# Kernel optimization log

Hardware: AMD Instinct MI355X
Metric: run time of the kernel (lower is better)

The kernel has to match this reference:

```python
import jax, jax.numpy as jnp
import numpy as np

N_HEADS = 32
D_MODEL = 1024
D_K = D_MODEL // N_HEADS  # 32; must equal N_HEADS for the module's broadcast to be valid
B, S = 2, 2048


def setup_inputs() -> dict:
    key = jax.random.key(0)
    ks = jax.random.split(key, 6)
    s = 0.02
    return {
        "x": jax.random.normal(ks[0], (B, S, D_MODEL), jnp.float32),
        "Wq": jax.random.normal(ks[1], (D_MODEL, D_MODEL), jnp.float32) * s,
        "bq": jnp.zeros((D_MODEL,), jnp.float32),
        "Wk": jax.random.normal(ks[2], (D_MODEL, D_K), jnp.float32) * s,
        "bk": jnp.zeros((D_K,), jnp.float32),
        "Wv": jax.random.normal(ks[3], (D_MODEL, D_K), jnp.float32) * s,
        "bv": jnp.zeros((D_K,), jnp.float32),
        "Wo": jax.random.normal(ks[4], (D_MODEL, D_MODEL), jnp.float32) * s,
        "bo": jnp.zeros((D_MODEL,), jnp.float32),
    }


def reference(x, Wq, bq, Wk, bk, Wv, bv, Wo, bo):
    b, s_len, d = x.shape
    q = x @ Wq + bq                 # (B,S,D)
    k = x @ Wk + bk                 # (B,S,D_K) -- single shared K head (MQA)
    v = x @ Wv + bv                 # (B,S,D_K)
    # Faithful to torch: view(B,S,d_k,n_heads).transpose(1,2) -> (B, D_K, S, N_HEADS)
    # The 'a' axis (size D_K) acts as the broadcast batch axis paired with the
    # expanded K/V head axis (size N_HEADS); valid because D_K == N_HEADS.
    q = q.reshape(b, s_len, D_K, N_HEADS).transpose(0, 2, 1, 3)  # (B,A,S,H)
    scores = jnp.einsum('bash,bth->bast', q, k) / jnp.sqrt(jnp.float32(D_K))  # (B,A,S,S)
    w = jax.nn.softmax(scores, axis=-1)
    out = jnp.einsum('bast,bte->base', w, v)  # (B,A,S,D_K)
    out = out.transpose(0, 2, 1, 3).reshape(b, s_len, d)  # (B,S,D)
    return out @ Wo + bo
```

## Files before the change

kernel.cpp:

```cpp
#include <hip/hip_runtime.h>
#include <cstdint>
#include <cstddef>

typedef unsigned short u16;
typedef unsigned int u32;
typedef __attribute__((ext_vector_type(8))) short short8;
typedef __attribute__((ext_vector_type(4))) float f32x4;

#define S_LEN 2048
#define NBATCH 2
#define DM 1024
#define DK 32
#define NH 32
#define M_ROWS 4096
#define SCALE 0.17677669529663687f

__device__ __forceinline__ u16 bf16_rne(float f) {
  u32 u = __float_as_uint(f);
  u32 r = (u + 0x7FFFu + ((u >> 16) & 1u)) >> 16;
  return (u16)r;
}
__device__ __forceinline__ void split2(float x, u16& hi, u16& lo) {
  u32 u = __float_as_uint(x);
  hi = (u16)(u >> 16);
  float hif = __uint_as_float(u & 0xFFFF0000u);
  lo = bf16_rne(x - hif);
}
__device__ __forceinline__ u32 pack2(float lo, float hi) {
  return (u32)bf16_rne(lo) | ((u32)bf16_rne(hi) << 16);
}

__global__ __launch_bounds__(256)
void split_x(const float* __restrict__ X, u16* __restrict__ Hi,
             u16* __restrict__ Lo) {
  const size_t i0 = ((size_t)blockIdx.x * 256 + threadIdx.x) * 8;
  const float4 v0 = *(const float4*)(X + i0);
  const float4 v1 = *(const float4*)(X + i0 + 4);
  const float f[8] = {v0.x, v0.y, v0.z, v0.w, v1.x, v1.y, v1.z, v1.w};
  u16 h[8], l[8];
#pragma unroll
  for (int e = 0; e < 8; ++e) split2(f[e], h[e], l[e]);
  uint4 hv, lv;
  hv.x = h[0] | ((u32)h[1] << 16); hv.y = h[2] | ((u32)h[3] << 16);
  hv.z = h[4] | ((u32)h[5] << 16); hv.w = h[6] | ((u32)h[7] << 16);
  lv.x = l[0] | ((u32)l[1] << 16); lv.y = l[2] | ((u32)l[3] << 16);
  lv.z = l[4] | ((u32)l[5] << 16); lv.w = l[6] | ((u32)l[7] << 16);
  *(uint4*)(Hi + i0) = hv;
  *(uint4*)(Lo + i0) = lv;
}

__global__ __launch_bounds__(256)
void tsplit(const float* __restrict__ W, u16* __restrict__ Thi,
            u16* __restrict__ Tlo) {
  __shared__ float tile[32][33];
  const int k0 = blockIdx.x * 32, n0 = blockIdx.y * 32;
  const int tx = threadIdx.x & 31, ty = threadIdx.x >> 5;
#pragma unroll
  for (int i = 0; i < 4; ++i)
    tile[ty + 8 * i][tx] = W[(size_t)(k0 + ty + 8 * i) * DM + n0 + tx];
  __syncthreads();
#pragma unroll
  for (int i = 0; i < 4; ++i) {
    const float v = tile[tx][ty + 8 * i];
    u16 h, l;
    split2(v, h, l);
    const size_t d = (size_t)(n0 + ty + 8 * i) * DM + k0 + tx;
    Thi[d] = h;
    Tlo[d] = l;
  }
}

template <int QMODE>
__global__ __launch_bounds__(256)
void gemm_mfma(const u16* __restrict__ Ahi, const u16* __restrict__ Alo,
               const u16* __restrict__ Bhi, const u16* __restrict__ Blo,
               const float* __restrict__ bias, float* __restrict__ C,
               u16* __restrict__ Ohi, u16* __restrict__ Olo) {
  __shared__ u16 lds[4][8][64][8];
  const int t = threadIdx.x;
  const int bid = blockIdx.x;
  const int swz = (bid & 7) * 32 + (bid >> 3);
  const int m0 = (swz & 31) * 128;
  const int n0 = (swz >> 5) * 128;

  const int r = t >> 1, h = t & 1;
  const size_t arow = (size_t)(m0 + r) * DM;
  const size_t brow = (size_t)(n0 + r) * DM;
  const int koff = 16 * h;
  const int mt = r >> 4;
  const int l0w = 32 * h + (r & 15);

  const int wr = t >> 7, wc = (t >> 6) & 1, l = t & 63;

  f32x4 acc[4][4];
#pragma unroll
  for (int i = 0; i < 4; ++i)
#pragma unroll
    for (int j = 0; j < 4; ++j) acc[i][j] = (f32x4){0.f, 0.f, 0.f, 0.f};

  int4 rah0, rah1, ral0, ral1, rbh0, rbh1, rbl0, rbl1;
#define GLOAD(k0)                                        \
  do {                                                   \
    const u16* pa = Ahi + arow + (k0) + koff;            \
    rah0 = *(const int4*)pa;                             \
    rah1 = *(const int4*)(pa + 8);                       \
    const u16* pal = Alo + arow + (k0) + koff;           \
    ral0 = *(const int4*)pal;                            \
    ral1 = *(const int4*)(pal + 8);                      \
    const u16* pb = Bhi + brow + (k0) + koff;            \
    rbh0 = *(const int4*)pb;                             \
    rbh1 = *(const int4*)(pb + 8);                       \
    const u16* pbl = Blo + brow + (k0) + koff;           \
    rbl0 = *(const int4*)pbl;                            \
    rbl1 = *(const int4*)(pbl + 8);                      \
  } while (0)

  GLOAD(0);

  for (int ks = 0; ks < 32; ++ks) {
    *(int4*)&lds[0][mt][l0w][0] = rah0;
    *(int4*)&lds[0][mt][l0w + 16][0] = rah1;
    *(int4*)&lds[1][mt][l0w][0] = ral0;
    *(int4*)&lds[1][mt][l0w + 16][0] = ral1;
    *(int4*)&lds[2][mt][l0w][0] = rbh0;
    *(int4*)&lds[2][mt][l0w + 16][0] = rbh1;
    *(int4*)&lds[3][mt][l0w][0] = rbl0;
    *(int4*)&lds[3][mt][l0w + 16][0] = rbl1;
    __syncthreads();
    if (ks < 31) GLOAD((ks + 1) * 32);

    short8 ah[4], al[4], bh[4], bl[4];
#pragma unroll
    for (int i = 0; i < 4; ++i) {
      ah[i] = *(const short8*)&lds[0][wr * 4 + i][l][0];
      al[i] = *(const short8*)&lds[1][wr * 4 + i][l][0];
      bh[i] = *(const short8*)&lds[2][wc * 4 + i][l][0];
      bl[i] = *(const short8*)&lds[3][wc * 4 + i][l][0];
    }
#pragma unroll
    for (int i = 0; i < 4; ++i)
#pragma unroll
      for (int j = 0; j < 4; ++j) {
        acc[i][j] = __builtin_amdgcn_mfma_f32_16x16x32_bf16(ah[i], bh[j],
                                                            acc[i][j], 0, 0, 0);
        acc[i][j] = __builtin_amdgcn_mfma_f32_16x16x32_bf16(ah[i], bl[j],
                                                            acc[i][j], 0, 0, 0);
        acc[i][j] = __builtin_amdgcn_mfma_f32_16x16x32_bf16(al[i], bh[j],
                                                            acc[i][j], 0, 0, 0);
      }
    __syncthreads();
  }
#undef GLOAD

  const int lcol = l & 15;
  float bj[4];
#pragma unroll
  for (int j = 0; j < 4; ++j) bj[j] = bias[n0 + wc * 64 + j * 16 + lcol];
#pragma unroll
  for (int i = 0; i < 4; ++i) {
    const int row0 = m0 + wr * 64 + i * 16 + (l >> 4) * 4;
#pragma unroll
    for (int j = 0; j < 4; ++j) {
      const int coln = n0 + wc * 64 + j * 16 + lcol;
#pragma unroll
      for (int q = 0; q < 4; ++q) {
        const float val = acc[i][j][q] + bj[j];
        if constexpr (QMODE == 0) {
          C[(size_t)(row0 + q) * DM + coln] = val;
        } else {
          u16 hh, ll;
          split2(val * SCALE, hh, ll);
          Ohi[(size_t)(row0 + q) * DM + coln] = hh;
          Olo[(size_t)(row0 + q) * DM + coln] = ll;
        }
      }
    }
  }
}

__global__ __launch_bounds__(256)
void kv_proj(const float* __restrict__ X, const float* __restrict__ Wk,
             const float* __restrict__ bk, const float* __restrict__ Wv,
             const float* __restrict__ bv, u16* __restrict__ Khi,
             u16* __restrict__ Klo, u16* __restrict__ Vthi,
             u16* __restrict__ Vtlo) {
  const int col = threadIdx.x & 63;
  const int rr = threadIdx.x >> 6;
  const int row = blockIdx.x * 4 + rr;
  const float* __restrict__ xr = X + (size_t)row * DM;
  const bool isK = col < DK;
  const int cc = isK ? col : col - DK;
  const float* __restrict__ w = (isK ? Wk : Wv) + cc;
  float acc = isK ? bk[cc] : bv[cc];
#pragma unroll 8
  for (int k = 0; k < DM; ++k) acc = fmaf(xr[k], w[(size_t)k * DK], acc);
  u16 h, l;
  split2(acc, h, l);
  if (isK) {
    Khi[(size_t)row * DK + cc] = h;
    Klo[(size_t)row * DK + cc] = l;
  } else {
    const size_t d =
        (size_t)(row >> 11) * DK * S_LEN + (size_t)cc * S_LEN + (row & 2047);
    Vthi[d] = h;
    Vtlo[d] = l;
  }
}

__global__ __launch_bounds__(256, 4)
void flash_mfma(const u16* __restrict__ Qhi, const u16* __restrict__ Qlo,
                const u16* __restrict__ Khi, const u16* __restrict__ Klo,
                const u16* __restrict__ Vthi, const u16* __restrict__ Vtlo,
                u16* __restrict__ Ohi, u16* __restrict__ Olo) {
  __shared__ u16 stg[4][2][64][8];
  __shared__ u16 plds[4][2][64][8];
  const int a = blockIdx.y, b = blockIdx.z;
  const int tid = threadIdx.x;
  const int wv = tid >> 6, l = tid & 63;
  const int lq = l & 15, lc = l >> 4;
  const int q0w = blockIdx.x * 128 + wv * 32;

  short8 qh[2], ql[2];
#pragma unroll
  for (int mt = 0; mt < 2; ++mt) {
    const size_t off =
        (size_t)(b * S_LEN + q0w + mt * 16 + lq) * DM + a * DK + lc * 8;
    qh[mt] = *(const short8*)(Qhi + off);
    ql[mt] = *(const short8*)(Qlo + off);
  }

  f32x4 oacc[2][2];
#pragma unroll
  for (int mt = 0; mt < 2; ++mt)
#pragma unroll
    for (int et = 0; et < 2; ++et) oacc[mt][et] = (f32x4){0.f, 0.f, 0.f, 0.f};
  float lsum[2] = {0.f, 0.f};

  const int g = tid & 127, sr = g >> 2, sc = g & 3;
  const u16* __restrict__ srcK =
      (tid < 128 ? Khi : Klo) + (size_t)(b * S_LEN + sr) * DK + sc * 8;
  const u16* __restrict__ srcV = (tid < 128 ? Vthi : Vtlo) +
                                 (size_t)b * DK * S_LEN + (size_t)sr * S_LEN +
                                 sc * 8;
  u16* const dstK = &stg[tid >> 7][sr >> 4][(sc << 4) | (sr & 15)][0];
  u16* const dstV = &stg[2 + (tid >> 7)][sr >> 4][(sc << 4) | (sr & 15)][0];

  int4 regK = *(const int4*)srcK;
  int4 regV = *(const int4*)srcV;

  for (int it = 0; it < 64; ++it) {
    *(int4*)dstK = regK;
    *(int4*)dstV = regV;
    __syncthreads();
    if (it < 63) {
      const int t0n = (it + 1) * 32;
      regK = *(const int4*)(srcK + (size_t)t0n * DK);
      regV = *(const int4*)(srcV + t0n);
    }
    short8 kh[2], kl[2], vh[2], vl[2];
#pragma unroll
    for (int tt = 0; tt < 2; ++tt) {
      kh[tt] = *(const short8*)&stg[0][tt][l][0];
      kl[tt] = *(const short8*)&stg[1][tt][l][0];
      vh[tt] = *(const short8*)&stg[2][tt][l][0];
      vl[tt] = *(const short8*)&stg[3][tt][l][0];
    }
#pragma unroll
    for (int mt = 0; mt < 2; ++mt) {
      f32x4 s0 = (f32x4){0.f, 0.f, 0.f, 0.f};
      f32x4 s1 = (f32x4){0.f, 0.f, 0.f, 0.f};
      s0 = __builtin_amdgcn_mfma_f32_16x16x32_bf16(kh[0], qh[mt], s0, 0, 0, 0);
      s0 = __builtin_amdgcn_mfma_f32_16x16x32_bf16(kh[0], ql[mt], s0, 0, 0, 0);
      s0 = __builtin_amdgcn_mfma_f32_16x16x32_bf16(kl[0], qh[mt], s0, 0, 0, 0);
      s1 = __builtin_amdgcn_mfma_f32_16x16x32_bf16(kh[1], qh[mt], s1, 0, 0, 0);
      s1 = __builtin_amdgcn_mfma_f32_16x16x32_bf16(kh[1], ql[mt], s1, 0, 0, 0);
      s1 = __builtin_amdgcn_mfma_f32_16x16x32_bf16(kl[1], qh[mt], s1, 0, 0, 0);
      const float e0 = __expf(s0[0]), e1 = __expf(s0[1]);
      const float e2 = __expf(s0[2]), e3 = __expf(s0[3]);
      const float e4 = __expf(s1[0]), e5 = __expf(s1[1]);
      const float e6 = __expf(s1[2]), e7 = __expf(s1[3]);
      lsum[mt] += ((e0 + e1) + (e2 + e3)) + ((e4 + e5) + (e6 + e7));
      const u32 pA = pack2(e0, e1), pB = pack2(e2, e3);
      const u32 pC = pack2(e4, e5), pD = pack2(e6, e7);
      const int fl1 = ((lc >> 1) << 4) | lq;
      const int fl2 = (((lc >> 1) + 2) << 4) | lq;
      *(uint2*)&plds[wv][mt][fl1][(lc & 1) * 4] = make_uint2(pA, pB);
      *(uint2*)&plds[wv][mt][fl2][(lc & 1) * 4] = make_uint2(pC, pD);
    }
    __syncthreads();
#pragma unroll
    for (int mt = 0; mt < 2; ++mt) {
      const short8 pf = *(const short8*)&plds[wv][mt][l][0];
      oacc[mt][0] = __builtin_amdgcn_mfma_f32_16x16x32_bf16(pf, vh[0],
                                                            oacc[mt][0], 0, 0, 0);
      oacc[mt][0] = __builtin_amdgcn_mfma_f32_16x16x32_bf16(pf, vl[0],
                                                            oacc[mt][0], 0, 0, 0);
      oacc[mt][1] = __builtin_amdgcn_mfma_f32_16x16x32_bf16(pf, vh[1],
                                                            oacc[mt][1], 0, 0, 0);
      oacc[mt][1] = __builtin_amdgcn_mfma_f32_16x16x32_bf16(pf, vl[1],
                                                            oacc[mt][1], 0, 0, 0);
    }
  }

#pragma unroll
  for (int mt = 0; mt < 2; ++mt) {
    float s = lsum[mt];
    s += __shfl_xor(s, 16);
    s += __shfl_xor(s, 32);
    const float inv = 1.f / s;
    float invr[4];
#pragma unroll
    for (int rg = 0; rg < 4; ++rg)
      invr[rg] = __int_as_float(__builtin_amdgcn_ds_bpermute(
          (((lc << 2) | rg)) << 2, __float_as_int(inv)));
    const size_t rb = (size_t)(b * S_LEN + q0w + mt * 16 + lc * 4);
#pragma unroll
    for (int et = 0; et < 2; ++et) {
#pragma unroll
      for (int rg = 0; rg < 4; ++rg) {
        const float val = oacc[mt][et][rg] * invr[rg];
        u16 hh, ll;
        split2(val, hh, ll);
        const size_t idx = (rb + rg) * DM + a * DK + et * 16 + lq;
        Ohi[idx] = hh;
        Olo[idx] = ll;
      }
    }
  }
}

extern "C" void kernel_launch(void* const* d_in, const int* in_sizes, int n_in,
                              void* d_out, int out_size, void* d_ws,
                              size_t ws_size, hipStream_t stream) {
  const float* x  = (const float*)d_in[0];
  const float* Wq = (const float*)d_in[1];
  const float* bq = (const float*)d_in[2];
  const float* Wk = (const float*)d_in[3];
  const float* bk = (const float*)d_in[4];
  const float* Wv = (const float*)d_in[5];
  const float* bv = (const float*)d_in[6];
  const float* Wo = (const float*)d_in[7];
  const float* bo = (const float*)d_in[8];
  float* out = (float*)d_out;

  char* ws = (char*)d_ws;
  const size_t MB = 1024 * 1024;
  u16* Xhi = (u16*)ws;
  u16* Xlo = (u16*)(ws + 8 * MB);
  u16* Khi  = (u16*)(ws + 16 * MB);
  u16* Klo  = (u16*)(ws + 16 * MB + 256 * 1024);
  u16* Vthi = (u16*)(ws + 16 * MB + 512 * 1024);
  u16* Vtlo = (u16*)(ws + 16 * MB + 768 * 1024);
  u16* Wqthi = (u16*)(ws + 17 * MB);
  u16* Wqtlo = (u16*)(ws + 19 * MB);
  u16* Wothi = (u16*)(ws + 21 * MB);
  u16* Wotlo = (u16*)(ws + 23 * MB);
  u16* Qhi = (u16*)d_out;
  u16* Qlo = Qhi + (size_t)M_ROWS * DM;

  hipLaunchKernelGGL(split_x, dim3(2048), dim3(256), 0, stream, x, Xhi, Xlo);
  hipLaunchKernelGGL(tsplit, dim3(32, 32), dim3(256), 0, stream, Wq, Wqthi,
                     Wqtlo);
  hipLaunchKernelGGL(tsplit, dim3(32, 32), dim3(256), 0, stream, Wo, Wothi,
                     Wotlo);
  hipLaunchKernelGGL(kv_proj, dim3(M_ROWS / 4), dim3(256), 0, stream, x, Wk,
                     bk, Wv, bv, Khi, Klo, Vthi, Vtlo);
  hipLaunchKernelGGL(HIP_KERNEL_NAME(gemm_mfma<1>), dim3(256), dim3(256), 0,
                     stream, Xhi, Xlo, Wqthi, Wqtlo, bq, (float*)nullptr, Qhi,
                     Qlo);
  hipLaunchKernelGGL(flash_mfma, dim3(16, NH, NBATCH), dim3(256), 0, stream,
                     Qhi, Qlo, Khi, Klo, Vthi, Vtlo, Xhi, Xlo);
  hipLaunchKernelGGL(HIP_KERNEL_NAME(gemm_mfma<0>), dim3(256), dim3(256), 0,
                     stream, Xhi, Xlo, Wothi, Wotlo, bo, out, (u16*)nullptr,
                     (u16*)nullptr);
}
```

Baseline: 350.4 us.

## Use direct global-to-LDS loads with double buffering in GEMM and attention kernels

```diff
diff --git a/kernel.cpp b/kernel.cpp
--- a/kernel.cpp
+++ b/kernel.cpp
@@ -28,6 +28,9 @@
 }
 __device__ __forceinline__ u32 pack2(float lo, float hi) {
   return (u32)bf16_rne(lo) | ((u32)bf16_rne(hi) << 16);
+}
+__device__ __forceinline__ void gl16(const u16* gsrc, u16* ldst) {
+  __builtin_amdgcn_global_load_lds((const u32*)gsrc, (u32*)ldst, 16, 0, 0);
 }
 
 __global__ __launch_bounds__(256)
@@ -71,97 +74,86 @@
 }
 
 template <int QMODE>
-__global__ __launch_bounds__(256)
-void gemm_mfma(const u16* __restrict__ Ahi, const u16* __restrict__ Alo,
-               const u16* __restrict__ Bhi, const u16* __restrict__ Blo,
-               const float* __restrict__ bias, float* __restrict__ C,
-               u16* __restrict__ Ohi, u16* __restrict__ Olo) {
-  __shared__ u16 lds[4][8][64][8];
+__global__ __launch_bounds__(256, 2)
+void gemm2(const u16* __restrict__ Ahi, const u16* __restrict__ Alo,
+           const u16* __restrict__ Bhi, const u16* __restrict__ Blo,
+           const float* __restrict__ bias, float* __restrict__ C,
+           u16* __restrict__ Ohi, u16* __restrict__ Olo) {
+  __shared__ u16 ldsA[2][2][8][64][8];
+  __shared__ u16 ldsB[2][2][4][64][8];
   const int t = threadIdx.x;
+  const int wvi = t >> 6, l = t & 63;
   const int bid = blockIdx.x;
-  const int swz = (bid & 7) * 32 + (bid >> 3);
-  const int m0 = (swz & 31) * 128;
-  const int n0 = (swz >> 5) * 128;
-
-  const int r = t >> 1, h = t & 1;
-  const size_t arow = (size_t)(m0 + r) * DM;
-  const size_t brow = (size_t)(n0 + r) * DM;
-  const int koff = 16 * h;
-  const int mt = r >> 4;
-  const int l0w = 32 * h + (r & 15);
-
-  const int wr = t >> 7, wc = (t >> 6) & 1, l = t & 63;
-
-  f32x4 acc[4][4];
+  const int wg = ((bid & 7) << 6) | (bid >> 3);
+  const int m0 = (wg >> 4) * 128;
+  const int n0 = (wg & 15) * 64;
+  const int wr = wvi >> 1, wc = wvi & 1;
+  const int lrow = l & 15, lk = (l >> 4) * 8;
+
+  const u16* sbase =
+      (wvi == 0) ? Ahi : (wvi == 1) ? Alo : (wvi == 2) ? Bhi : Blo;
+  const int srow0 = (wvi < 2) ? m0 : n0;
+
+  f32x4 acc[4][2];
 #pragma unroll
   for (int i = 0; i < 4; ++i)
 #pragma unroll
-    for (int j = 0; j < 4; ++j) acc[i][j] = (f32x4){0.f, 0.f, 0.f, 0.f};
-
-  int4 rah0, rah1, ral0, ral1, rbh0, rbh1, rbl0, rbl1;
-#define GLOAD(k0)                                        \
-  do {                                                   \
-    const u16* pa = Ahi + arow + (k0) + koff;            \
-    rah0 = *(const int4*)pa;                             \
-    rah1 = *(const int4*)(pa + 8);                       \
-    const u16* pal = Alo + arow + (k0) + koff;           \
-    ral0 = *(const int4*)pal;                            \
-    ral1 = *(const int4*)(pal + 8);                      \
-    const u16* pb = Bhi + brow + (k0) + koff;            \
-    rbh0 = *(const int4*)pb;                             \
-    rbh1 = *(const int4*)(pb + 8);                       \
-    const u16* pbl = Blo + brow + (k0) + koff;           \
-    rbl0 = *(const int4*)pbl;                            \
-    rbl1 = *(const int4*)(pbl + 8);                      \
-  } while (0)
-
-  GLOAD(0);
-
+    for (int j = 0; j < 2; ++j) acc[i][j] = (f32x4){0.f, 0.f, 0.f, 0.f};
+
+  auto issue = [&](int buf, int kk) {
+    if (wvi < 2) {
+#pragma unroll
+      for (int mt = 0; mt < 8; ++mt)
+        gl16(sbase + (size_t)(srow0 + mt * 16 + lrow) * DM + kk + lk,
+             &ldsA[buf][wvi][mt][0][0]);
+    } else {
+#pragma unroll
+      for (int nt = 0; nt < 4; ++nt)
+        gl16(sbase + (size_t)(srow0 + nt * 16 + lrow) * DM + kk + lk,
+             &ldsB[buf][wvi - 2][nt][0][0]);
+    }
+  };
+
+  issue(0, 0);
   for (int ks = 0; ks < 32; ++ks) {
-    *(int4*)&lds[0][mt][l0w][0] = rah0;
-    *(int4*)&lds[0][mt][l0w + 16][0] = rah1;
-    *(int4*)&lds[1][mt][l0w][0] = ral0;
-    *(int4*)&lds[1][mt][l0w + 16][0] = ral1;
-    *(int4*)&lds[2][mt][l0w][0] = rbh0;
-    *(int4*)&lds[2][mt][l0w + 16][0] = rbh1;
-    *(int4*)&lds[3][mt][l0w][0] = rbl0;
-    *(int4*)&lds[3][mt][l0w + 16][0] = rbl1;
+    const int cb = ks & 1;
     __syncthreads();
-    if (ks < 31) GLOAD((ks + 1) * 32);
-
-    short8 ah[4], al[4], bh[4], bl[4];
+    if (ks < 31) issue(cb ^ 1, (ks + 1) * 32);
+
+    short8 ah[4], alo[4], bh[2], bl[2];
 #pragma unroll
     for (int i = 0; i < 4; ++i) {
-      ah[i] = *(const short8*)&lds[0][wr * 4 + i][l][0];
-      al[i] = *(const short8*)&lds[1][wr * 4 + i][l][0];
-      bh[i] = *(const short8*)&lds[2][wc * 4 + i][l][0];
-      bl[i] = *(const short8*)&lds[3][wc * 4 + i][l][0];
+      ah[i] = *(const short8*)&ldsA[cb][0][wr * 4 + i][l][0];
+      alo[i] = *(const short8*)&ldsA[cb][1][wr * 4 + i][l][0];
+    }
+#pragma unroll
+    for (int j = 0; j < 2; ++j) {
+      bh[j] = *(const short8*)&ldsB[cb][0][wc * 2 + j][l][0];
+      bl[j] = *(const short8*)&ldsB[cb][1][wc * 2 + j][l][0];
     }
 #pragma unroll
     for (int i = 0; i < 4; ++i)
 #pragma unroll
-      for (int j = 0; j < 4; ++j) {
+      for (int j = 0; j < 2; ++j) {
         acc[i][j] = __builtin_amdgcn_mfma_f32_16x16x32_bf16(ah[i], bh[j],
                                                             acc[i][j], 0, 0, 0);
         acc[i][j] = __builtin_amdgcn_mfma_f32_16x16x32_bf16(ah[i], bl[j],
                                                             acc[i][j], 0, 0, 0);
-        acc[i][j] = __builtin_amdgcn_mfma_f32_16x16x32_bf16(al[i], bh[j],
+        acc[i][j] = __builtin_amdgcn_mfma_f32_16x16x32_bf16(alo[i], bh[j],
                                                             acc[i][j], 0, 0, 0);
       }
-    __syncthreads();
-  }
-#undef GLOAD
+  }
 
   const int lcol = l & 15;
-  float bj[4];
-#pragma unroll
-  for (int j = 0; j < 4; ++j) bj[j] = bias[n0 + wc * 64 + j * 16 + lcol];
+  float bj[2];
+#pragma unroll
+  for (int j = 0; j < 2; ++j) bj[j] = bias[n0 + wc * 32 + j * 16 + lcol];
 #pragma unroll
   for (int i = 0; i < 4; ++i) {
     const int row0 = m0 + wr * 64 + i * 16 + (l >> 4) * 4;
 #pragma unroll
-    for (int j = 0; j < 4; ++j) {
-      const int coln = n0 + wc * 64 + j * 16 + lcol;
+    for (int j = 0; j < 2; ++j) {
+      const int coln = n0 + wc * 32 + j * 16 + lcol;
 #pragma unroll
       for (int q = 0; q < 4; ++q) {
         const float val = acc[i][j][q] + bj[j];
@@ -208,17 +200,19 @@
 }
 
 __global__ __launch_bounds__(256, 4)
-void flash_mfma(const u16* __restrict__ Qhi, const u16* __restrict__ Qlo,
-                const u16* __restrict__ Khi, const u16* __restrict__ Klo,
-                const u16* __restrict__ Vthi, const u16* __restrict__ Vtlo,
-                u16* __restrict__ Ohi, u16* __restrict__ Olo) {
-  __shared__ u16 stg[4][2][64][8];
+void flash_mfma2(const u16* __restrict__ Qhi, const u16* __restrict__ Qlo,
+                 const u16* __restrict__ Khi, const u16* __restrict__ Klo,
+                 const u16* __restrict__ Vthi, const u16* __restrict__ Vtlo,
+                 u16* __restrict__ Ohi, u16* __restrict__ Olo) {
+  __shared__ u16 stg[2][4][2][64][8];
   __shared__ u16 plds[4][2][64][8];
   const int a = blockIdx.y, b = blockIdx.z;
   const int tid = threadIdx.x;
   const int wv = tid >> 6, l = tid & 63;
   const int lq = l & 15, lc = l >> 4;
   const int q0w = blockIdx.x * 128 + wv * 32;
+  const size_t bS = (size_t)b * S_LEN;
+  const size_t bDS = (size_t)b * DK * S_LEN;
 
   short8 qh[2], ql[2];
 #pragma unroll
@@ -236,34 +230,36 @@
     for (int et = 0; et < 2; ++et) oacc[mt][et] = (f32x4){0.f, 0.f, 0.f, 0.f};
   float lsum[2] = {0.f, 0.f};
 
-  const int g = tid & 127, sr = g >> 2, sc = g & 3;
-  const u16* __restrict__ srcK =
-      (tid < 128 ? Khi : Klo) + (size_t)(b * S_LEN + sr) * DK + sc * 8;
-  const u16* __restrict__ srcV = (tid < 128 ? Vthi : Vtlo) +
-                                 (size_t)b * DK * S_LEN + (size_t)sr * S_LEN +
-                                 sc * 8;
-  u16* const dstK = &stg[tid >> 7][sr >> 4][(sc << 4) | (sr & 15)][0];
-  u16* const dstV = &stg[2 + (tid >> 7)][sr >> 4][(sc << 4) | (sr & 15)][0];
-
-  int4 regK = *(const int4*)srcK;
-  int4 regV = *(const int4*)srcV;
-
+  const u16* kbase = (wv == 0) ? Khi : Klo;
+  const u16* vbase = (wv == 2) ? Vthi : Vtlo;
+
+  auto issue = [&](int buf, int t0) {
+    if (wv < 2) {
+#pragma unroll
+      for (int tt = 0; tt < 2; ++tt)
+        gl16(kbase + (bS + t0 + tt * 16 + lq) * DK + lc * 8,
+             &stg[buf][wv][tt][0][0]);
+    } else {
+#pragma unroll
+      for (int tt = 0; tt < 2; ++tt)
+        gl16(vbase + bDS + (size_t)(tt * 16 + lq) * S_LEN + t0 + lc * 8,
+             &stg[buf][wv][tt][0][0]);
+    }
+  };
+
+  issue(0, 0);
   for (int it = 0; it < 64; ++it) {
-    *(int4*)dstK = regK;
-    *(int4*)dstV = regV;
+    const int cb = it & 1;
     __syncthreads();
-    if (it < 63) {
-      const int t0n = (it + 1) * 32;
-      regK = *(const int4*)(srcK + (size_t)t0n * DK);
-      regV = *(const int4*)(srcV + t0n);
-    }
-    short8 kh[2], kl[2], vh[2], vl[2];
+    if (it < 63) issue(cb ^ 1, (it + 1) * 32);
+
+    short8 kh[2], klo[2], vh[2], vl[2];
 #pragma unroll
     for (int tt = 0; tt < 2; ++tt) {
-      kh[tt] = *(const short8*)&stg[0][tt][l][0];
-      kl[tt] = *(const short8*)&stg[1][tt][l][0];
-      vh[tt] = *(const short8*)&stg[2][tt][l][0];
-      vl[tt] = *(const short8*)&stg[3][tt][l][0];
+      kh[tt] = *(const short8*)&stg[cb][0][tt][l][0];
+      klo[tt] = *(const short8*)&stg[cb][1][tt][l][0];
+      vh[tt] = *(const short8*)&stg[cb][2][tt][l][0];
+      vl[tt] = *(const short8*)&stg[cb][3][tt][l][0];
     }
 #pragma unroll
     for (int mt = 0; mt < 2; ++mt) {
@@ -271,10 +267,10 @@
       f32x4 s1 = (f32x4){0.f, 0.f, 0.f, 0.f};
       s0 = __builtin_amdgcn_mfma_f32_16x16x32_bf16(kh[0], qh[mt], s0, 0, 0, 0);
       s0 = __builtin_amdgcn_mfma_f32_16x16x32_bf16(kh[0], ql[mt], s0, 0, 0, 0);
-      s0 = __builtin_amdgcn_mfma_f32_16x16x32_bf16(kl[0], qh[mt], s0, 0, 0, 0);
+      s0 = __builtin_amdgcn_mfma_f32_16x16x32_bf16(klo[0], qh[mt], s0, 0, 0, 0);
       s1 = __builtin_amdgcn_mfma_f32_16x16x32_bf16(kh[1], qh[mt], s1, 0, 0, 0);
       s1 = __builtin_amdgcn_mfma_f32_16x16x32_bf16(kh[1], ql[mt], s1, 0, 0, 0);
-      s1 = __builtin_amdgcn_mfma_f32_16x16x32_bf16(kl[1], qh[mt], s1, 0, 0, 0);
+      s1 = __builtin_amdgcn_mfma_f32_16x16x32_bf16(klo[1], qh[mt], s1, 0, 0, 0);
       const float e0 = __expf(s0[0]), e1 = __expf(s0[1]);
       const float e2 = __expf(s0[2]), e3 = __expf(s0[3]);
       const float e4 = __expf(s1[0]), e5 = __expf(s1[1]);
@@ -287,7 +283,6 @@
       *(uint2*)&plds[wv][mt][fl1][(lc & 1) * 4] = make_uint2(pA, pB);
       *(uint2*)&plds[wv][mt][fl2][(lc & 1) * 4] = make_uint2(pC, pD);
     }
-    __syncthreads();
 #pragma unroll
     for (int mt = 0; mt < 2; ++mt) {
       const short8 pf = *(const short8*)&plds[wv][mt][l][0];
@@ -365,12 +360,12 @@
                      Wotlo);
   hipLaunchKernelGGL(kv_proj, dim3(M_ROWS / 4), dim3(256), 0, stream, x, Wk,
                      bk, Wv, bv, Khi, Klo, Vthi, Vtlo);
-  hipLaunchKernelGGL(HIP_KERNEL_NAME(gemm_mfma<1>), dim3(256), dim3(256), 0,
+  hipLaunchKernelGGL(HIP_KERNEL_NAME(gemm2<1>), dim3(512), dim3(256), 0,
                      stream, Xhi, Xlo, Wqthi, Wqtlo, bq, (float*)nullptr, Qhi,
                      Qlo);
-  hipLaunchKernelGGL(flash_mfma, dim3(16, NH, NBATCH), dim3(256), 0, stream,
+  hipLaunchKernelGGL(flash_mfma2, dim3(16, NH, NBATCH), dim3(256), 0, stream,
                      Qhi, Qlo, Khi, Klo, Vthi, Vtlo, Xhi, Xlo);
-  hipLaunchKernelGGL(HIP_KERNEL_NAME(gemm_mfma<0>), dim3(256), dim3(256), 0,
+  hipLaunchKernelGGL(HIP_KERNEL_NAME(gemm2<0>), dim3(512), dim3(256), 0,
                      stream, Xhi, Xlo, Wothi, Wotlo, bo, out, (u16*)nullptr,
                      (u16*)nullptr);
 }
```

Result: no change. 348.9 us (-0.4%).
